# Kernel tuning notes

Hardware: AMD Instinct MI355X
Metric: run time of the kernel (lower is better)

Reference implementation:

```python
import jax, jax.numpy as jnp
import numpy as np

V, CTX, D, L, H = 50257, 2048, 768, 12, 12
HD = D // H
EPS = 1e-5


def _ln(x, w, b):
    mu = jnp.mean(x, axis=-1, keepdims=True)
    var = jnp.mean(jnp.square(x - mu), axis=-1, keepdims=True)
    return (x - mu) * jax.lax.rsqrt(var + EPS) * w + b


def setup_inputs() -> dict:
    key = jax.random.key(0)
    ks = jax.random.split(key, 8)
    s = 0.02  # init std, matches _init_weights
    return {
        "idx": jax.random.randint(ks[0], (2, 2048), 0, V),
        "wte": jax.random.normal(ks[1], (V, D), jnp.float32) * s,
        "wpe": jax.random.normal(ks[2], (CTX, D), jnp.float32) * s,
        "ln1_w": jnp.ones((L, D), jnp.float32),
        "ln1_b": jnp.zeros((L, D), jnp.float32),
        "qkv_w": jax.random.normal(ks[3], (L, 3 * D, D), jnp.float32) * s,
        "out_w": jax.random.normal(ks[4], (L, D, D), jnp.float32) * s,
        "ln2_w": jnp.ones((L, D), jnp.float32),
        "ln2_b": jnp.zeros((L, D), jnp.float32),
        "fc1_w": jax.random.normal(ks[5], (L, 4 * D, D), jnp.float32) * s,
        "fc2_w": jax.random.normal(ks[6], (L, D, 4 * D), jnp.float32) * s,
        "lnf_w": jnp.ones((D,), jnp.float32),
        "lnf_b": jnp.zeros((D,), jnp.float32),
    }


def reference(idx, wte, wpe, ln1_w, ln1_b, qkv_w, out_w, ln2_w, ln2_b,
              fc1_w, fc2_w, lnf_w, lnf_b):
    B, S = idx.shape
    x = wte[idx] + wpe[:S][None]  # [B,S,D]
    causal = jnp.tril(jnp.ones((S, S), bool))  # [S,S]
    scale = 1.0 / np.sqrt(HD)

    def block(x, p):
        l1w, l1b, qkvw, ow, l2w, l2b, f1w, f2w = p
        h = _ln(x, l1w, l1b)
        qkv = h @ qkvw.T  # [B,S,3D]
        q, k, v = jnp.split(qkv, 3, axis=-1)
        q = q.reshape(B, S, H, HD)
        k = k.reshape(B, S, H, HD)
        v = v.reshape(B, S, H, HD)
        scores = jnp.einsum("bqhd,bkhd->bhqk", q, k) * scale
        scores = jnp.where(causal, scores, -jnp.inf)
        attn = jax.nn.softmax(scores, axis=-1)
        ctx = jnp.einsum("bhqk,bkhd->bqhd", attn, v).reshape(B, S, D)
        x = x + ctx @ ow.T
        h2 = _ln(x, l2w, l2b)
        mlp = jax.nn.gelu(h2 @ f1w.T, approximate=False) @ f2w.T
        return x + mlp, None

    x, _ = jax.lax.scan(block, x, (ln1_w, ln1_b, qkv_w, out_w, ln2_w, ln2_b, fc1_w, fc2_w))
    x = _ln(x, lnf_w, lnf_b)
    logits = x @ wte.T  # tied lm_head
    return logits
```

## Files before the change

### kernel.cpp

```cpp
#include <hip/hip_runtime.h>
#include <hip/hip_bf16.h>
#include <math.h>

typedef __attribute__((ext_vector_type(4))) float f32x4;
typedef __attribute__((ext_vector_type(8))) short bf16x8;
typedef __attribute__((ext_vector_type(4))) float float4v;
typedef unsigned short u16;
typedef unsigned int u32;

#define DIM 768
#define SEQ 2048
#define NTOK 4096
#define NH 12
#define NL 12
#define VOCAB 50257

__device__ __forceinline__ u16 f2bf(float f) {
  union { float f; u32 u; } c; c.f = f;
  u32 u = c.u;
  u32 r = u + 0x7fffu + ((u >> 16) & 1u);
  return (u16)(r >> 16);
}

__device__ __forceinline__ float fexp2(float x) {
#if __has_builtin(__builtin_amdgcn_exp2f)
  return __builtin_amdgcn_exp2f(x);
#else
  return exp2f(x);
#endif
}

__device__ __forceinline__ f32x4 mfma_bf16(bf16x8 a, bf16x8 b, f32x4 c) {
  return __builtin_amdgcn_mfma_f32_16x16x32_bf16(a, b, c, 0, 0, 0);
}

__device__ __forceinline__ void gload_lds16(const u16* g, u16* l) {
  __builtin_amdgcn_global_load_lds((const __attribute__((address_space(1))) u32*)g,
                                   (__attribute__((address_space(3))) u32*)l, 16, 0, 0);
}

__global__ void embed_k(const int* __restrict__ idx, const float* __restrict__ wte,
                        const float* __restrict__ wpe, float* __restrict__ x) {
  int t = blockIdx.x * 256 + threadIdx.x;
  int n = t / 192, c = t % 192;
  int tok = idx[n];
  float4v a = ((const float4v*)wte)[(size_t)tok * 192 + c];
  float4v p = ((const float4v*)wpe)[(size_t)(n & (SEQ - 1)) * 192 + c];
  ((float4v*)x)[t] = a + p;
}

__global__ __launch_bounds__(256) void ln_k(const float* __restrict__ x,
                                            const float* __restrict__ w,
                                            const float* __restrict__ b,
                                            u16* __restrict__ out) {
  int lane = threadIdx.x & 63;
  int row = blockIdx.x * 4 + (threadIdx.x >> 6);
  const float4v* xr = (const float4v*)(x + (size_t)row * DIM);
  float4v v[3];
#pragma unroll
  for (int i = 0; i < 3; ++i) v[i] = xr[i * 64 + lane];
  float s = 0.f;
#pragma unroll
  for (int i = 0; i < 3; ++i)
#pragma unroll
    for (int j = 0; j < 4; ++j) s += v[i][j];
#pragma unroll
  for (int o = 1; o < 64; o <<= 1) s += __shfl_xor(s, o);
  float mu = s * (1.f / 768.f);
  float vs = 0.f;
#pragma unroll
  for (int i = 0; i < 3; ++i)
#pragma unroll
    for (int j = 0; j < 4; ++j) { float d = v[i][j] - mu; vs += d * d; }
#pragma unroll
  for (int o = 1; o < 64; o <<= 1) vs += __shfl_xor(vs, o);
  float rs = rsqrtf(vs * (1.f / 768.f) + 1e-5f);
  u16* orow = out + (size_t)row * DIM;
#pragma unroll
  for (int i = 0; i < 3; ++i) {
    float4v wv = ((const float4v*)w)[i * 64 + lane];
    float4v bv = ((const float4v*)b)[i * 64 + lane];
    float y0 = (v[i][0] - mu) * rs * wv[0] + bv[0];
    float y1 = (v[i][1] - mu) * rs * wv[1] + bv[1];
    float y2 = (v[i][2] - mu) * rs * wv[2] + bv[2];
    float y3 = (v[i][3] - mu) * rs * wv[3] + bv[3];
    uint2 pk;
    pk.x = (u32)f2bf(y0) | ((u32)f2bf(y1) << 16);
    pk.y = (u32)f2bf(y2) | ((u32)f2bf(y3) << 16);
    ((uint2*)orow)[i * 64 + lane] = pk;
  }
}

__global__ void cvt_k(const float* __restrict__ src, u16* __restrict__ dst, int n4) {
  int stride = gridDim.x * blockDim.x;
  for (int i = blockIdx.x * blockDim.x + threadIdx.x; i < n4; i += stride) {
    float4v v = ((const float4v*)src)[i];
    uint2 pk;
    pk.x = (u32)f2bf(v[0]) | ((u32)f2bf(v[1]) << 16);
    pk.y = (u32)f2bf(v[2]) | ((u32)f2bf(v[3]) << 16);
    ((uint2*)dst)[i] = pk;
  }
}

template <int EPI>
__global__ __launch_bounds__(256) void gemm_bt(const u16* __restrict__ A,
                                               const u16* __restrict__ W, int Mdim,
                                               int Kdim, u16* __restrict__ outb,
                                               float* __restrict__ resid) {
  __shared__ u16 lA[128 * 64];
  __shared__ u16 lW[128 * 64];
  const int m0 = blockIdx.y * 128;
  const int n0 = blockIdx.x * 128;
  const int tid = threadIdx.x;
  const int lane = tid & 63, wv = tid >> 6;
  const int wr = wv >> 1, wc = wv & 1;
  const int lr = lane & 15, hi = lane >> 4;

  f32x4 acc[4][4];
#pragma unroll
  for (int i = 0; i < 4; ++i)
#pragma unroll
    for (int j = 0; j < 4; ++j) acc[i][j] = (f32x4){0.f, 0.f, 0.f, 0.f};

  const int s_row = tid >> 3;
  const int s_col = (tid & 7) * 8;
  int wrow[4];
#pragma unroll
  for (int it = 0; it < 4; ++it) {
    int r = m0 + s_row + it * 32;
    wrow[it] = (r < Mdim) ? r : (Mdim - 1);
  }

  for (int k0 = 0; k0 < Kdim; k0 += 64) {
    __syncthreads();
#pragma unroll
    for (int it = 0; it < 4; ++it) {
      gload_lds16(A + (size_t)(n0 + s_row + it * 32) * Kdim + k0 + s_col,
                  &lA[(s_row + it * 32) * 64 + s_col]);
      gload_lds16(W + (size_t)wrow[it] * Kdim + k0 + s_col,
                  &lW[(s_row + it * 32) * 64 + s_col]);
    }
    __syncthreads();
#pragma unroll
    for (int kk = 0; kk < 2; ++kk) {
      bf16x8 af[4], wf[4];
#pragma unroll
      for (int i = 0; i < 4; ++i)
        af[i] = *(const bf16x8*)(&lA[(wr * 64 + i * 16 + lr) * 64 + kk * 32 + hi * 8]);
#pragma unroll
      for (int j = 0; j < 4; ++j)
        wf[j] = *(const bf16x8*)(&lW[(wc * 64 + j * 16 + lr) * 64 + kk * 32 + hi * 8]);
#pragma unroll
      for (int i = 0; i < 4; ++i)
#pragma unroll
        for (int j = 0; j < 4; ++j) acc[i][j] = mfma_bf16(af[i], wf[j], acc[i][j]);
    }
  }

#pragma unroll
  for (int i = 0; i < 4; ++i) {
#pragma unroll
    for (int j = 0; j < 4; ++j) {
      int nb = n0 + wr * 64 + i * 16 + hi * 4;
      int m = m0 + wc * 64 + j * 16 + lr;
#pragma unroll
      for (int r = 0; r < 4; ++r) {
        float val = acc[i][j][r];
        size_t o = (size_t)(nb + r) * Mdim + m;
        if (EPI == 0) {
          if (m < Mdim) outb[o] = f2bf(val);
        } else if (EPI == 1) {
          float g = 0.5f * val * (1.f + erff(val * 0.70710678118f));
          outb[o] = f2bf(g);
        } else if (EPI == 2) {
          resid[o] += val;
        } else {
          if (m < Mdim) resid[o] = val;
        }
      }
    }
  }
}

template <int EPI>
__global__ __launch_bounds__(512) void gemm256(const u16* __restrict__ A,
                                               const u16* __restrict__ W, int Mdim,
                                               int Kdim, u16* __restrict__ outb,
                                               float* __restrict__ resid) {
  __shared__ u16 lA[2][256 * 64];
  __shared__ u16 lB[2][256 * 64];
  const int n0 = blockIdx.x * 256;
  const int m0 = blockIdx.y * 256;
  const int tid = threadIdx.x;
  const int lane = tid & 63, wid = tid >> 6;
  const int wr = wid >> 2, wc = wid & 3;
  const int lr = lane & 15, hi = lane >> 4;

  const int s_row = tid >> 3;
  const int s_col = (tid & 7) * 8;
  const int g_col = s_col ^ ((s_row & 7) << 3);
  int wrow[4];
#pragma unroll
  for (int it = 0; it < 4; ++it) {
    int r = m0 + s_row + it * 64;
    wrow[it] = (r < Mdim) ? r : (Mdim - 1);
  }

  f32x4 acc[8][4];
#pragma unroll
  for (int i = 0; i < 8; ++i)
#pragma unroll
    for (int j = 0; j < 4; ++j) acc[i][j] = (f32x4){0.f, 0.f, 0.f, 0.f};

  const int nt = Kdim >> 6;

  auto stage = [&](int kt, int buf) {
    const int k0 = kt * 64;
#pragma unroll
    for (int it = 0; it < 4; ++it)
      gload_lds16(A + (size_t)(n0 + s_row + it * 64) * Kdim + k0 + g_col,
                  &lA[buf][(s_row + it * 64) * 64 + s_col]);
#pragma unroll
    for (int it = 0; it < 4; ++it)
      gload_lds16(W + (size_t)wrow[it] * Kdim + k0 + g_col,
                  &lB[buf][(s_row + it * 64) * 64 + s_col]);
  };

  const int swz = (lr & 7) << 3;

  stage(0, 0);
  stage(1, 1);
  asm volatile("s_waitcnt vmcnt(8)" ::: "memory");
  __builtin_amdgcn_s_barrier();

  for (int t = 0; t < nt; ++t) {
    const int cur = t & 1;
    const u16* la = lA[cur];
    const u16* lb = lB[cur];
#pragma unroll
    for (int kk = 0; kk < 2; ++kk) {
      const int csw = (kk * 32 + hi * 8) ^ swz;
      bf16x8 af[8], wf[4];
#pragma unroll
      for (int i = 0; i < 8; ++i)
        af[i] = *(const bf16x8*)(&la[(wr * 128 + i * 16 + lr) * 64 + csw]);
#pragma unroll
      for (int j = 0; j < 4; ++j)
        wf[j] = *(const bf16x8*)(&lb[(wc * 64 + j * 16 + lr) * 64 + csw]);
      __builtin_amdgcn_s_setprio(1);
#pragma unroll
      for (int i = 0; i < 8; ++i)
#pragma unroll
        for (int j = 0; j < 4; ++j) acc[i][j] = mfma_bf16(af[i], wf[j], acc[i][j]);
      __builtin_amdgcn_s_setprio(0);
    }
    __builtin_amdgcn_s_barrier();
    if (t + 2 < nt) {
      stage(t + 2, cur);
      asm volatile("s_waitcnt vmcnt(8)" ::: "memory");
    } else if (t + 1 < nt) {
      asm volatile("s_waitcnt vmcnt(0)" ::: "memory");
    }
    __builtin_amdgcn_s_barrier();
  }

#pragma unroll
  for (int i = 0; i < 8; ++i) {
#pragma unroll
    for (int j = 0; j < 4; ++j) {
      int nb = n0 + wr * 128 + i * 16 + hi * 4;
      int m = m0 + wc * 64 + j * 16 + lr;
#pragma unroll
      for (int r = 0; r < 4; ++r) {
        float val = acc[i][j][r];
        size_t o = (size_t)(nb + r) * Mdim + m;
        if (EPI == 0) {
          if (m < Mdim) outb[o] = f2bf(val);
        } else if (EPI == 1) {
          float g = 0.5f * val * (1.f + erff(val * 0.70710678118f));
          outb[o] = f2bf(g);
        } else {
          if (m < Mdim) resid[o] = val;
        }
      }
    }
  }
}

__global__ __launch_bounds__(256) void vtrans_k(const u16* __restrict__ qkv,
                                                u16* __restrict__ vT) {
  __shared__ u16 t[64][65];
  int bh = blockIdx.y;
  int b = bh / NH, h = bh % NH;
  int s0 = blockIdx.x * 64;
  int tid = threadIdx.x;
  int col = tid & 63, row0 = tid >> 6;
#pragma unroll
  for (int it = 0; it < 16; ++it) {
    int srow = row0 + it * 4;
    t[srow][col] = qkv[(size_t)(b * SEQ + s0 + srow) * 2304 + 1536 + h * 64 + col];
  }
  __syncthreads();
#pragma unroll
  for (int it = 0; it < 16; ++it) {
    int drow = row0 + it * 4;
    vT[((size_t)bh * 64 + drow) * SEQ + s0 + col] = t[col][drow];
  }
}

__global__ __launch_bounds__(512) void flash_k(const u16* __restrict__ qkv,
                                               const u16* __restrict__ vT,
                                               u16* __restrict__ ctx) {
  const int tid = threadIdx.x;
  const int lane = tid & 63, wq = tid >> 6;
  const int lr = lane & 15, hi = lane >> 4;
  const int pi = blockIdx.x;
  const int bh = blockIdx.y;
  const int b = bh / NH, h = bh % NH;
  const size_t rowb = (size_t)b * SEQ;
  const float SCL = 0.125f * 1.44269504f;

  __shared__ u16 lK[64 * 80];
  __shared__ u16 lV[64 * 80];
  __shared__ u16 Pb[8][16 * 40];
  u16* P = Pb[wq];

  const int s_row = tid >> 3;
  const int s_col = (tid & 7) * 8;
  const u16* kSrc = qkv + rowb * 2304 + 768 + h * 64;
  const u16* vSrc = vT + ((size_t)bh * 64 + s_row) * SEQ;

#pragma unroll
  for (int pass = 0; pass < 2; ++pass) {
    const int qb = (pass == 0 ? (15 - pi) : pi) * 128;
    const int qa = qb + wq * 16;

    const u16* Qp = qkv + (rowb + qa + lr) * 2304 + h * 64 + hi * 8;
    bf16x8 qf0 = *(const bf16x8*)(Qp);
    bf16x8 qf1 = *(const bf16x8*)(Qp + 32);

    f32x4 o[4];
    float mreg[4], lreg[4];
#pragma unroll
    for (int ct = 0; ct < 4; ++ct) o[ct] = (f32x4){0.f, 0.f, 0.f, 0.f};
#pragma unroll
    for (int r = 0; r < 4; ++r) { mreg[r] = -1e30f; lreg[r] = 0.f; }

    const int kTop = qb + 127;
    bf16x8 kreg = *(const bf16x8*)(kSrc + (size_t)s_row * 2304 + s_col);
    bf16x8 vreg = *(const bf16x8*)(vSrc + s_col);

    for (int k0 = 0; k0 <= kTop; k0 += 64) {
      __syncthreads();
      *(bf16x8*)(&lK[s_row * 80 + s_col]) = kreg;
      *(bf16x8*)(&lV[s_row * 80 + s_col]) = vreg;
      __syncthreads();
      if (k0 + 64 <= kTop) {
        kreg = *(const bf16x8*)(kSrc + (size_t)(k0 + 64 + s_row) * 2304 + s_col);
        vreg = *(const bf16x8*)(vSrc + k0 + 64 + s_col);
      }
      if (k0 <= qa + 15) {
#pragma unroll
        for (int ks = 0; ks < 2; ++ks) {
          const int kg = k0 + ks * 32;
          f32x4 s0 = (f32x4){0.f, 0.f, 0.f, 0.f}, s1 = (f32x4){0.f, 0.f, 0.f, 0.f};
          {
            bf16x8 ka = *(const bf16x8*)(&lK[(ks * 32 + lr) * 80 + hi * 8]);
            bf16x8 kc = *(const bf16x8*)(&lK[(ks * 32 + lr) * 80 + hi * 8 + 32]);
            s0 = mfma_bf16(qf0, ka, s0);
            s0 = mfma_bf16(qf1, kc, s0);
            bf16x8 kd = *(const bf16x8*)(&lK[(ks * 32 + 16 + lr) * 80 + hi * 8]);
            bf16x8 ke = *(const bf16x8*)(&lK[(ks * 32 + 16 + lr) * 80 + hi * 8 + 32]);
            s1 = mfma_bf16(qf0, kd, s1);
            s1 = mfma_bf16(qf1, ke, s1);
          }
          float cor[4];
#pragma unroll
          for (int r = 0; r < 4; ++r) {
            int qrow = qa + hi * 4 + r;
            float v0 = s0[r] * SCL;
            if (kg + lr > qrow) v0 = -1e30f;
            float v1 = s1[r] * SCL;
            if (kg + 16 + lr > qrow) v1 = -1e30f;
            s0[r] = v0; s1[r] = v1;
            float m = fmaxf(v0, v1);
            m = fmaxf(m, __shfl_xor(m, 1));
            m = fmaxf(m, __shfl_xor(m, 2));
            m = fmaxf(m, __shfl_xor(m, 4));
            m = fmaxf(m, __shfl_xor(m, 8));
            float mnew = fmaxf(mreg[r], m);
            cor[r] = fexp2(mreg[r] - mnew);
            mreg[r] = mnew;
          }
#pragma unroll
          for (int r = 0; r < 4; ++r) {
            float p0 = fexp2(s0[r] - mreg[r]);
            float p1 = fexp2(s1[r] - mreg[r]);
            lreg[r] = lreg[r] * cor[r] + p0 + p1;
            P[(hi * 4 + r) * 40 + lr] = f2bf(p0);
            P[(hi * 4 + r) * 40 + 16 + lr] = f2bf(p1);
#pragma unroll
            for (int ct = 0; ct < 4; ++ct) o[ct][r] *= cor[r];
          }
          bf16x8 pa = *(const bf16x8*)(&P[lr * 40 + hi * 8]);
#pragma unroll
          for (int ct = 0; ct < 4; ++ct) {
            bf16x8 vf = *(const bf16x8*)(&lV[(ct * 16 + lr) * 80 + ks * 32 + hi * 8]);
            o[ct] = mfma_bf16(pa, vf, o[ct]);
          }
        }
      }
    }

    float lfin[4];
#pragma unroll
    for (int r = 0; r < 4; ++r) {
      float l = lreg[r];
      l += __shfl_xor(l, 1);
      l += __shfl_xor(l, 2);
      l += __shfl_xor(l, 4);
      l += __shfl_xor(l, 8);
      lfin[r] = 1.f / l;
    }
#pragma unroll
    for (int ct = 0; ct < 4; ++ct)
#pragma unroll
      for (int r = 0; r < 4; ++r) {
        float ov = o[ct][r] * lfin[r];
        size_t n = rowb + qa + hi * 4 + r;
        ctx[n * DIM + h * 64 + ct * 16 + lr] = f2bf(ov);
      }
  }
}

extern "C" void kernel_launch(void* const* d_in, const int* in_sizes, int n_in,
                              void* d_out, int out_size, void* d_ws, size_t ws_size,
                              hipStream_t stream) {
  (void)in_sizes; (void)n_in; (void)out_size; (void)ws_size;
  const int* idx = (const int*)d_in[0];
  const float* wte = (const float*)d_in[1];
  const float* wpe = (const float*)d_in[2];
  const float* ln1w = (const float*)d_in[3];
  const float* ln1b = (const float*)d_in[4];
  const float* qkvw = (const float*)d_in[5];
  const float* outw = (const float*)d_in[6];
  const float* ln2w = (const float*)d_in[7];
  const float* ln2b = (const float*)d_in[8];
  const float* fc1w = (const float*)d_in[9];
  const float* fc2w = (const float*)d_in[10];
  const float* lnfw = (const float*)d_in[11];
  const float* lnfb = (const float*)d_in[12];
  float* out = (float*)d_out;

  char* ws = (char*)d_ws;
  size_t off = 0;
  auto carve = [&](size_t bytes) {
    char* p = ws + off;
    off += (bytes + 255) & ~(size_t)255;
    return p;
  };
  u16* hb = (u16*)carve((size_t)NTOK * DIM * 2);
  u16* wteb = (u16*)carve((size_t)VOCAB * DIM * 2);

  char* os = (char*)d_out;
  size_t ooff = 0;
  auto ocarve = [&](size_t bytes) {
    char* p = os + ooff;
    ooff += (bytes + 255) & ~(size_t)255;
    return p;
  };
  float* xb = (float*)ocarve((size_t)NTOK * DIM * 4);
  u16* qkvb = (u16*)ocarve((size_t)NTOK * 3 * DIM * 2);
  u16* ctxb = (u16*)ocarve((size_t)NTOK * DIM * 2);
  u16* mhb = (u16*)ocarve((size_t)NTOK * 4 * DIM * 2);
  u16* vTb = (u16*)ocarve((size_t)2 * NH * 64 * SEQ * 2);
  u16* qkvwb = (u16*)ocarve((size_t)NL * 1769472 * 2);
  u16* outwb = (u16*)ocarve((size_t)NL * 589824 * 2);
  u16* fc1wb = (u16*)ocarve((size_t)NL * 2359296 * 2);
  u16* fc2wb = (u16*)ocarve((size_t)NL * 2359296 * 2);

  cvt_k<<<2048, 256, 0, stream>>>(qkvw, qkvwb, NL * 442368);
  cvt_k<<<2048, 256, 0, stream>>>(outw, outwb, NL * 147456);
  cvt_k<<<2048, 256, 0, stream>>>(fc1w, fc1wb, NL * 589824);
  cvt_k<<<2048, 256, 0, stream>>>(fc2w, fc2wb, NL * 589824);
  cvt_k<<<2048, 256, 0, stream>>>(wte, wteb, 9649344);

  embed_k<<<3072, 256, 0, stream>>>(idx, wte, wpe, xb);

  for (int l = 0; l < NL; ++l) {
    ln_k<<<1024, 256, 0, stream>>>(xb, ln1w + l * DIM, ln1b + l * DIM, hb);
    gemm256<0><<<dim3(16, 9), 512, 0, stream>>>(hb, qkvwb + (size_t)l * 1769472,
                                                2304, 768, qkvb, nullptr);
    vtrans_k<<<dim3(32, 24), 256, 0, stream>>>(qkvb, vTb);
    flash_k<<<dim3(8, 24), 512, 0, stream>>>(qkvb, vTb, ctxb);
    gemm_bt<2><<<dim3(32, 6), 256, 0, stream>>>(ctxb, outwb + (size_t)l * 589824,
                                                768, 768, nullptr, xb);
    ln_k<<<1024, 256, 0, stream>>>(xb, ln2w + l * DIM, ln2b + l * DIM, hb);
    gemm256<1><<<dim3(16, 12), 512, 0, stream>>>(hb, fc1wb + (size_t)l * 2359296,
                                                 3072, 768, mhb, nullptr);
    gemm_bt<2><<<dim3(32, 6), 256, 0, stream>>>(mhb, fc2wb + (size_t)l * 2359296,
                                                768, 3072, nullptr, xb);
  }

  ln_k<<<1024, 256, 0, stream>>>(xb, lnfw, lnfb, hb);
  gemm256<3><<<dim3(16, 197), 512, 0, stream>>>(hb, wteb, VOCAB, 768, nullptr, out);
}
```

Before: 4.042 ms.

## Use 128-key K/V tiles and 64-key softmax steps with conditional rescale in flash attention

Loads 128 keys of K and V into shared memory per barrier pair instead of 64, and processes each 64-key half with four score MFMAs per step instead of two. The online-softmax max reduction and rescale now run once per 64 keys, and the accumulator rescale is skipped when no row's running max increased. This is meant to cut barrier, shuffle and exp overhead per key, at the cost of more shared memory, more registers and a divergent branch.

```diff
diff --git a/kernel.cpp b/kernel.cpp
--- a/kernel.cpp
+++ b/kernel.cpp
@@ -320,9 +320,9 @@
   const size_t rowb = (size_t)b * SEQ;
   const float SCL = 0.125f * 1.44269504f;
 
-  __shared__ u16 lK[64 * 80];
-  __shared__ u16 lV[64 * 80];
-  __shared__ u16 Pb[8][16 * 40];
+  __shared__ u16 lK[128 * 80];
+  __shared__ u16 lV[64 * 136];
+  __shared__ u16 Pb[8][16 * 76];
   u16* P = Pb[wq];
 
   const int s_row = tid >> 3;
@@ -346,68 +346,91 @@
 #pragma unroll
     for (int r = 0; r < 4; ++r) { mreg[r] = -1e30f; lreg[r] = 0.f; }
 
-    const int kTop = qb + 127;
-    bf16x8 kreg = *(const bf16x8*)(kSrc + (size_t)s_row * 2304 + s_col);
-    bf16x8 vreg = *(const bf16x8*)(vSrc + s_col);
-
-    for (int k0 = 0; k0 <= kTop; k0 += 64) {
+    const int kEnd = qb + 128;
+    bf16x8 kr0 = *(const bf16x8*)(kSrc + (size_t)s_row * 2304 + s_col);
+    bf16x8 kr1 = *(const bf16x8*)(kSrc + (size_t)(s_row + 64) * 2304 + s_col);
+    bf16x8 vr0 = *(const bf16x8*)(vSrc + s_col);
+    bf16x8 vr1 = *(const bf16x8*)(vSrc + 64 + s_col);
+
+    for (int k0 = 0; k0 < kEnd; k0 += 128) {
       __syncthreads();
-      *(bf16x8*)(&lK[s_row * 80 + s_col]) = kreg;
-      *(bf16x8*)(&lV[s_row * 80 + s_col]) = vreg;
+      *(bf16x8*)(&lK[s_row * 80 + s_col]) = kr0;
+      *(bf16x8*)(&lK[(s_row + 64) * 80 + s_col]) = kr1;
+      *(bf16x8*)(&lV[s_row * 136 + s_col]) = vr0;
+      *(bf16x8*)(&lV[s_row * 136 + 64 + s_col]) = vr1;
       __syncthreads();
-      if (k0 + 64 <= kTop) {
-        kreg = *(const bf16x8*)(kSrc + (size_t)(k0 + 64 + s_row) * 2304 + s_col);
-        vreg = *(const bf16x8*)(vSrc + k0 + 64 + s_col);
+      if (k0 + 128 < kEnd) {
+        kr0 = *(const bf16x8*)(kSrc + (size_t)(k0 + 128 + s_row) * 2304 + s_col);
+        kr1 = *(const bf16x8*)(kSrc + (size_t)(k0 + 192 + s_row) * 2304 + s_col);
+        vr0 = *(const bf16x8*)(vSrc + k0 + 128 + s_col);
+        vr1 = *(const bf16x8*)(vSrc + k0 + 192 + s_col);
       }
-      if (k0 <= qa + 15) {
-#pragma unroll
-        for (int ks = 0; ks < 2; ++ks) {
-          const int kg = k0 + ks * 32;
-          f32x4 s0 = (f32x4){0.f, 0.f, 0.f, 0.f}, s1 = (f32x4){0.f, 0.f, 0.f, 0.f};
-          {
-            bf16x8 ka = *(const bf16x8*)(&lK[(ks * 32 + lr) * 80 + hi * 8]);
-            bf16x8 kc = *(const bf16x8*)(&lK[(ks * 32 + lr) * 80 + hi * 8 + 32]);
-            s0 = mfma_bf16(qf0, ka, s0);
-            s0 = mfma_bf16(qf1, kc, s0);
-            bf16x8 kd = *(const bf16x8*)(&lK[(ks * 32 + 16 + lr) * 80 + hi * 8]);
-            bf16x8 ke = *(const bf16x8*)(&lK[(ks * 32 + 16 + lr) * 80 + hi * 8 + 32]);
-            s1 = mfma_bf16(qf0, kd, s1);
-            s1 = mfma_bf16(qf1, ke, s1);
+#pragma unroll
+      for (int sub = 0; sub < 2; ++sub) {
+        const int kg = k0 + sub * 64;
+        if (kg > qa + 15) continue;
+        f32x4 s[4];
+#pragma unroll
+        for (int j = 0; j < 4; ++j) s[j] = (f32x4){0.f, 0.f, 0.f, 0.f};
+#pragma unroll
+        for (int j = 0; j < 4; ++j) {
+          const u16* kp = &lK[(sub * 64 + j * 16 + lr) * 80 + hi * 8];
+          bf16x8 ka = *(const bf16x8*)(kp);
+          bf16x8 kc = *(const bf16x8*)(kp + 32);
+          s[j] = mfma_bf16(qf0, ka, s[j]);
+          s[j] = mfma_bf16(qf1, kc, s[j]);
+        }
+        float mnew[4];
+        int grew = 0;
+#pragma unroll
+        for (int r = 0; r < 4; ++r) {
+          int qrow = qa + hi * 4 + r;
+#pragma unroll
+          for (int j = 0; j < 4; ++j) {
+            float v = s[j][r] * SCL;
+            if (kg + j * 16 + lr > qrow) v = -1e30f;
+            s[j][r] = v;
           }
-          float cor[4];
+          float m01 = fmaxf(fmaxf(s[0][r], s[1][r]), fmaxf(s[2][r], s[3][r]));
+          m01 = fmaxf(m01, __shfl_xor(m01, 1));
+          m01 = fmaxf(m01, __shfl_xor(m01, 2));
+          m01 = fmaxf(m01, __shfl_xor(m01, 4));
+          m01 = fmaxf(m01, __shfl_xor(m01, 8));
+          mnew[r] = fmaxf(mreg[r], m01);
+          grew |= (mnew[r] > mreg[r]) ? 1 : 0;
+        }
+        if (__any(grew)) {
 #pragma unroll
           for (int r = 0; r < 4; ++r) {
-            int qrow = qa + hi * 4 + r;
-            float v0 = s0[r] * SCL;
-            if (kg + lr > qrow) v0 = -1e30f;
-            float v1 = s1[r] * SCL;
-            if (kg + 16 + lr > qrow) v1 = -1e30f;
-            s0[r] = v0; s1[r] = v1;
-            float m = fmaxf(v0, v1);
-            m = fmaxf(m, __shfl_xor(m, 1));
-            m = fmaxf(m, __shfl_xor(m, 2));
-            m = fmaxf(m, __shfl_xor(m, 4));
-            m = fmaxf(m, __shfl_xor(m, 8));
-            float mnew = fmaxf(mreg[r], m);
-            cor[r] = fexp2(mreg[r] - mnew);
-            mreg[r] = mnew;
+            float c = fexp2(mreg[r] - mnew[r]);
+            lreg[r] *= c;
+#pragma unroll
+            for (int ct = 0; ct < 4; ++ct) o[ct][r] *= c;
+            mreg[r] = mnew[r];
           }
-#pragma unroll
-          for (int r = 0; r < 4; ++r) {
-            float p0 = fexp2(s0[r] - mreg[r]);
-            float p1 = fexp2(s1[r] - mreg[r]);
-            lreg[r] = lreg[r] * cor[r] + p0 + p1;
-            P[(hi * 4 + r) * 40 + lr] = f2bf(p0);
-            P[(hi * 4 + r) * 40 + 16 + lr] = f2bf(p1);
-#pragma unroll
-            for (int ct = 0; ct < 4; ++ct) o[ct][r] *= cor[r];
-          }
-          bf16x8 pa = *(const bf16x8*)(&P[lr * 40 + hi * 8]);
-#pragma unroll
-          for (int ct = 0; ct < 4; ++ct) {
-            bf16x8 vf = *(const bf16x8*)(&lV[(ct * 16 + lr) * 80 + ks * 32 + hi * 8]);
-            o[ct] = mfma_bf16(pa, vf, o[ct]);
-          }
+        }
+#pragma unroll
+        for (int r = 0; r < 4; ++r) {
+          float p0 = fexp2(s[0][r] - mreg[r]);
+          float p1 = fexp2(s[1][r] - mreg[r]);
+          float p2 = fexp2(s[2][r] - mreg[r]);
+          float p3 = fexp2(s[3][r] - mreg[r]);
+          lreg[r] += p0 + p1 + p2 + p3;
+          u16* pr = &P[(hi * 4 + r) * 76];
+          pr[lr] = f2bf(p0);
+          pr[16 + lr] = f2bf(p1);
+          pr[32 + lr] = f2bf(p2);
+          pr[48 + lr] = f2bf(p3);
+        }
+        bf16x8 pa0 = *(const bf16x8*)(&P[lr * 76 + hi * 8]);
+        bf16x8 pa1 = *(const bf16x8*)(&P[lr * 76 + 32 + hi * 8]);
+#pragma unroll
+        for (int ct = 0; ct < 4; ++ct) {
+          const u16* vp = &lV[(ct * 16 + lr) * 136 + sub * 64];
+          bf16x8 vf0 = *(const bf16x8*)(vp + hi * 8);
+          bf16x8 vf1 = *(const bf16x8*)(vp + 32 + hi * 8);
+          o[ct] = mfma_bf16(pa0, vf0, o[ct]);
+          o[ct] = mfma_bf16(pa1, vf1, o[ct]);
         }
       }
     }
```

New measurement: 4.091 ms. Within noise of the previous version (+1.2%).

## Double-buffer and swizzle LDS in 128-tile GEMM for out-proj and fc2

Applied to the files above, without the earlier changes.

The 128x128 GEMM used for the attention output projection and fc2 now uses two LDS buffers and prefetches tile t+2 while computing tile t, with vmcnt waits replacing the two full syncthreads per k-step. Global-load columns are XOR-swizzled by row so the fragment reads from LDS avoid bank conflicts, and s_setprio is raised around the MFMA burst. This is meant to hide global-load latency and LDS conflicts. In exchange the kernel uses twice the LDS, which may lower occupancy.

```diff
diff --git a/kernel.cpp b/kernel.cpp
--- a/kernel.cpp
+++ b/kernel.cpp
@@ -103,12 +103,12 @@
 }
 
 template <int EPI>
-__global__ __launch_bounds__(256) void gemm_bt(const u16* __restrict__ A,
-                                               const u16* __restrict__ W, int Mdim,
-                                               int Kdim, u16* __restrict__ outb,
-                                               float* __restrict__ resid) {
-  __shared__ u16 lA[128 * 64];
-  __shared__ u16 lW[128 * 64];
+__global__ __launch_bounds__(256) void gemm128p(const u16* __restrict__ A,
+                                                const u16* __restrict__ W, int Mdim,
+                                                int Kdim, u16* __restrict__ outb,
+                                                float* __restrict__ resid) {
+  __shared__ u16 lA[2][128 * 64];
+  __shared__ u16 lW[2][128 * 64];
   const int m0 = blockIdx.y * 128;
   const int n0 = blockIdx.x * 128;
   const int tid = threadIdx.x;
@@ -124,6 +124,7 @@
 
   const int s_row = tid >> 3;
   const int s_col = (tid & 7) * 8;
+  const int g_col = s_col ^ ((s_row & 7) << 3);
   int wrow[4];
 #pragma unroll
   for (int it = 0; it < 4; ++it) {
@@ -131,30 +132,55 @@
     wrow[it] = (r < Mdim) ? r : (Mdim - 1);
   }
 
-  for (int k0 = 0; k0 < Kdim; k0 += 64) {
-    __syncthreads();
+  const int nt = Kdim >> 6;
+
+  auto stage = [&](int kt, int buf) {
+    const int k0 = kt * 64;
 #pragma unroll
     for (int it = 0; it < 4; ++it) {
-      gload_lds16(A + (size_t)(n0 + s_row + it * 32) * Kdim + k0 + s_col,
-                  &lA[(s_row + it * 32) * 64 + s_col]);
-      gload_lds16(W + (size_t)wrow[it] * Kdim + k0 + s_col,
-                  &lW[(s_row + it * 32) * 64 + s_col]);
-    }
-    __syncthreads();
+      gload_lds16(A + (size_t)(n0 + s_row + it * 32) * Kdim + k0 + g_col,
+                  &lA[buf][(s_row + it * 32) * 64 + s_col]);
+      gload_lds16(W + (size_t)wrow[it] * Kdim + k0 + g_col,
+                  &lW[buf][(s_row + it * 32) * 64 + s_col]);
+    }
+  };
+
+  const int swz = (lr & 7) << 3;
+
+  stage(0, 0);
+  stage(1, 1);
+  asm volatile("s_waitcnt vmcnt(8)" ::: "memory");
+  __builtin_amdgcn_s_barrier();
+
+  for (int t = 0; t < nt; ++t) {
+    const int cur = t & 1;
+    const u16* la = lA[cur];
+    const u16* lw = lW[cur];
 #pragma unroll
     for (int kk = 0; kk < 2; ++kk) {
+      const int csw = (kk * 32 + hi * 8) ^ swz;
       bf16x8 af[4], wf[4];
 #pragma unroll
       for (int i = 0; i < 4; ++i)
-        af[i] = *(const bf16x8*)(&lA[(wr * 64 + i * 16 + lr) * 64 + kk * 32 + hi * 8]);
+        af[i] = *(const bf16x8*)(&la[(wr * 64 + i * 16 + lr) * 64 + csw]);
 #pragma unroll
       for (int j = 0; j < 4; ++j)
-        wf[j] = *(const bf16x8*)(&lW[(wc * 64 + j * 16 + lr) * 64 + kk * 32 + hi * 8]);
+        wf[j] = *(const bf16x8*)(&lw[(wc * 64 + j * 16 + lr) * 64 + csw]);
+      __builtin_amdgcn_s_setprio(1);
 #pragma unroll
       for (int i = 0; i < 4; ++i)
 #pragma unroll
         for (int j = 0; j < 4; ++j) acc[i][j] = mfma_bf16(af[i], wf[j], acc[i][j]);
-    }
+      __builtin_amdgcn_s_setprio(0);
+    }
+    __builtin_amdgcn_s_barrier();
+    if (t + 2 < nt) {
+      stage(t + 2, cur);
+      asm volatile("s_waitcnt vmcnt(8)" ::: "memory");
+    } else if (t + 1 < nt) {
+      asm volatile("s_waitcnt vmcnt(0)" ::: "memory");
+    }
+    __builtin_amdgcn_s_barrier();
   }
 
 #pragma unroll
@@ -493,13 +519,13 @@
                                                 2304, 768, qkvb, nullptr);
     vtrans_k<<<dim3(32, 24), 256, 0, stream>>>(qkvb, vTb);
     flash_k<<<dim3(8, 24), 512, 0, stream>>>(qkvb, vTb, ctxb);
-    gemm_bt<2><<<dim3(32, 6), 256, 0, stream>>>(ctxb, outwb + (size_t)l * 589824,
-                                                768, 768, nullptr, xb);
+    gemm128p<2><<<dim3(32, 6), 256, 0, stream>>>(ctxb, outwb + (size_t)l * 589824,
+                                                 768, 768, nullptr, xb);
     ln_k<<<1024, 256, 0, stream>>>(xb, ln2w + l * DIM, ln2b + l * DIM, hb);
     gemm256<1><<<dim3(16, 12), 512, 0, stream>>>(hb, fc1wb + (size_t)l * 2359296,
                                                  3072, 768, mhb, nullptr);
-    gemm_bt<2><<<dim3(32, 6), 256, 0, stream>>>(mhb, fc2wb + (size_t)l * 2359296,
-                                                768, 3072, nullptr, xb);
+    gemm128p<2><<<dim3(32, 6), 256, 0, stream>>>(mhb, fc2wb + (size_t)l * 2359296,
+                                                 768, 3072, nullptr, xb);
   }
 
   ln_k<<<1024, 256, 0, stream>>>(xb, lnfw, lnfb, hb);
```

Result: no change. 3.979 ms, median of 4 (-1.6%).
